# Optimization experiments

Measured on AMD Instinct MI355X. Metric: run time of the kernel, lower is better.

## Reference

```python
import jax, jax.numpy as jnp
import numpy as np

K = 10  # num_objects: top-k humans and top-k objects per image
PERSON_ID = 1
NEG = jnp.float32(-1e30)


def setup_inputs() -> dict:
    key = jax.random.key(0)
    B, N, h, w, D = 8, 100, 96, 96, 768
    kf, ks, k1, k2, k3 = jax.random.split(key, 5)
    features = jax.random.normal(kf, (B, h, w, D), dtype=jnp.float32)
    # valid integer boxes (x1,y1,x2,y2) with x2>x1, y2>y1, inside the feature grid
    rng = np.random.default_rng(0)
    x1 = rng.integers(0, w - 1, (B, N)); x2 = rng.integers(x1 + 1, w + 1)
    y1 = rng.integers(0, h - 1, (B, N)); y2 = rng.integers(y1 + 1, h + 1)
    boxes = jnp.asarray(np.stack([x1, y1, x2, y2], axis=-1).astype(np.int32))
    lab = rng.integers(2, 82, (B, N))
    lab = np.where(rng.random((B, N)) < 0.3, PERSON_ID, lab)
    labels = jnp.asarray(lab.astype(np.int32))
    scores = jax.random.uniform(ks, (B, N), dtype=jnp.float32)
    s = 0.02
    W1 = jax.random.normal(k1, (2 * D, 512), jnp.float32) * s
    b1 = jnp.zeros((512,), jnp.float32)
    W2 = jax.random.normal(k2, (512, 256), jnp.float32) * s
    b2 = jnp.zeros((256,), jnp.float32)
    W3 = jax.random.normal(k3, (256, 117), jnp.float32) * s
    b3 = jnp.zeros((117,), jnp.float32)
    return dict(features=features, boxes=boxes, labels=labels, scores=scores,
                W1=W1, b1=b1, W2=W2, b2=b2, W3=W3, b3=b3)


def _box_mean_pool(features, boxes):
    # Integral image (summed-area table) so all variable-size box means are one gather.
    B, h, w, D = features.shape
    sat = jnp.cumsum(jnp.cumsum(features, axis=1), axis=2)
    sat = jnp.pad(sat, ((0, 0), (1, 0), (1, 0), (0, 0)))  # [B,h+1,w+1,D]
    x1, y1, x2, y2 = boxes[..., 0], boxes[..., 1], boxes[..., 2], boxes[..., 3]
    bi = jnp.arange(B)[:, None]
    box_sum = (sat[bi, y2, x2] - sat[bi, y1, x2]
               - sat[bi, y2, x1] + sat[bi, y1, x1])          # [B,N,D]
    area = ((y2 - y1) * (x2 - x1)).astype(features.dtype)
    return box_sum / area[..., None]


def reference(features, boxes, labels, scores, W1, b1, W2, b2, W3, b3):
    B = features.shape[0]
    D = features.shape[-1]
    pooled = _box_mean_pool(features, boxes)                 # [B,N,D]
    # split by category and take top-K by score (== sort desc + truncate)
    h_sc = jnp.where(labels == PERSON_ID, scores, NEG)
    o_sc = jnp.where(labels != PERSON_ID, scores, NEG)
    hval, hidx = jax.lax.top_k(h_sc, K)                      # [B,K]
    oval, oidx = jax.lax.top_k(o_sc, K)
    h_ok = hval > NEG / 2
    o_ok = oval > NEG / 2
    hfeat = jnp.take_along_axis(pooled, hidx[..., None], axis=1)  # [B,K,D]
    ofeat = jnp.take_along_axis(pooled, oidx[..., None], axis=1)  # [B,K,D]
    # pairwise human-object concat -> [B,K,K,2D]
    pair = jnp.concatenate([
        jnp.broadcast_to(hfeat[:, :, None, :], (B, K, K, D)),
        jnp.broadcast_to(ofeat[:, None, :, :], (B, K, K, D)),
    ], axis=-1)
    x = jax.nn.relu(pair @ W1 + b1)
    x = jax.nn.relu(x @ W2 + b2)
    rel = x @ W3 + b3                                        # [B,K,K,117]
    valid = h_ok[:, :, None] & o_ok[:, None, :]              # [B,K,K] ragged mask
    rel = rel * valid[..., None].astype(rel.dtype)
    return rel, valid
```

## Files before the change

### kernel.cpp

```cpp
#include <hip/hip_runtime.h>
#include <math.h>

#define Bsz 8
#define NBOX 100
#define Hh 96
#define Ww 96
#define Dd 768
#define KK 10
#define C1 512
#define C2 256
#define C3 117

#define OFF_SELIDX 0
#define OFF_OK     160
#define OFF_INV    320
#define OFF_POOLED 512
#define OFF_PART   (512 + 160*Dd)

__global__ void topk_kernel(const int* __restrict__ labels,
                            const float* __restrict__ scores,
                            const int* __restrict__ boxes,
                            int* __restrict__ sel_idx,
                            float* __restrict__ sel_ok,
                            float* __restrict__ inv_area) {
    __shared__ float arr[16][NBOX];
    int tid = threadIdx.x;
    for (int idx = tid; idx < 16 * NBOX; idx += 64) {
        int t = idx / NBOX, n = idx % NBOX;
        int b = t >> 1, c = t & 1;
        int lab = labels[b * NBOX + n];
        bool is_h = (lab == 1);
        bool keep = (c == 0) ? is_h : !is_h;
        arr[t][n] = keep ? scores[b * NBOX + n] : -1e30f;
    }
    __syncthreads();
    if (tid >= 16) return;
    int t = tid, b = t >> 1, c = t & 1;
    for (int k = 0; k < KK; ++k) {
        float bv = -INFINITY; int bi = 0;
        for (int n = 0; n < NBOX; ++n) {
            float v = arr[t][n];
            if (v > bv) { bv = v; bi = n; }
        }
        arr[t][bi] = -INFINITY;
        int s = (b * 2 + c) * KK + k;
        sel_idx[s] = bi;
        sel_ok[s] = (bv > -5e29f) ? 1.0f : 0.0f;
        const int* bx = boxes + (b * NBOX + bi) * 4;
        float area = (float)((bx[3] - bx[1]) * (bx[2] - bx[0]));
        inv_area[s] = 1.0f / area;
    }
}

__global__ void pool_kernel(const float* __restrict__ feat,
                            const int* __restrict__ boxes,
                            const int* __restrict__ sel_idx,
                            float* __restrict__ pooled) {
    int s = blockIdx.x;
    int y = blockIdx.y;
    int b = s / (2 * KK);
    int n = sel_idx[s];
    const int* bx = boxes + (b * NBOX + n) * 4;
    int x1 = bx[0], y1 = bx[1], x2 = bx[2], y2 = bx[3];
    if (y < y1 || y >= y2) return;
    int d4 = threadIdx.x;
    const float4* rowp = (const float4*)feat
        + ((size_t)(b * Hh + y) * Ww) * (Dd / 4) + d4;
    float4 a0 = make_float4(0.f, 0.f, 0.f, 0.f);
    float4 a1 = a0, a2 = a0, a3 = a0;
    int x = x1;
    for (; x + 4 <= x2; x += 4) {
        float4 v0 = rowp[(size_t)(x + 0) * (Dd / 4)];
        float4 v1 = rowp[(size_t)(x + 1) * (Dd / 4)];
        float4 v2 = rowp[(size_t)(x + 2) * (Dd / 4)];
        float4 v3 = rowp[(size_t)(x + 3) * (Dd / 4)];
        a0.x += v0.x; a0.y += v0.y; a0.z += v0.z; a0.w += v0.w;
        a1.x += v1.x; a1.y += v1.y; a1.z += v1.z; a1.w += v1.w;
        a2.x += v2.x; a2.y += v2.y; a2.z += v2.z; a2.w += v2.w;
        a3.x += v3.x; a3.y += v3.y; a3.z += v3.z; a3.w += v3.w;
    }
    for (; x < x2; ++x) {
        float4 v0 = rowp[(size_t)x * (Dd / 4)];
        a0.x += v0.x; a0.y += v0.y; a0.z += v0.z; a0.w += v0.w;
    }
    a0.x += a1.x + a2.x + a3.x;
    a0.y += a1.y + a2.y + a3.y;
    a0.z += a1.z + a2.z + a3.z;
    a0.w += a1.w + a2.w + a3.w;
    float* dst = &pooled[(size_t)s * Dd + d4 * 4];
    atomicAdd(dst + 0, a0.x);
    atomicAdd(dst + 1, a0.y);
    atomicAdd(dst + 2, a0.z);
    atomicAdd(dst + 3, a0.w);
}

__global__ void part_kernel(const float* __restrict__ pooled,
                            const float* __restrict__ inv_area,
                            const float* __restrict__ W1,
                            float* __restrict__ part) {
    __shared__ float pv[KK * Dd];
    int sg = blockIdx.x;
    int o = blockIdx.y * 256 + threadIdx.x;
    for (int idx = threadIdx.x; idx < KK * Dd; idx += 256)
        pv[idx] = pooled[(size_t)sg * KK * Dd + idx];
    __syncthreads();
    int c = sg & 1;
    const float* Wp = W1 + (size_t)(c * Dd) * C1 + o;
    float acc[KK];
#pragma unroll
    for (int j = 0; j < KK; ++j) acc[j] = 0.f;
    for (int d = 0; d < Dd; ++d) {
        float w = Wp[(size_t)d * C1];
#pragma unroll
        for (int j = 0; j < KK; ++j) acc[j] += pv[j * Dd + d] * w;
    }
    for (int j = 0; j < KK; ++j)
        part[(size_t)(sg * KK + j) * C1 + o] = acc[j] * inv_area[sg * KK + j];
}

__global__ void mlp_kernel(const float* __restrict__ part,
                           const float* __restrict__ sel_ok,
                           const float* __restrict__ b1,
                           const float* __restrict__ W2,
                           const float* __restrict__ b2,
                           const float* __restrict__ W3,
                           const float* __restrict__ b3,
                           float* __restrict__ out) {
    __shared__ float x1s[KK][C1];
    __shared__ float x2s[KK][C2];
    int blk = blockIdx.x;
    int b = blk / KK, i = blk % KK;
    const float* hp = part + (size_t)(b * 2 * KK + i) * C1;
    const float* op = part + (size_t)(b * 2 * KK + KK) * C1;
    int tid = threadIdx.x;

    for (int o = tid; o < C1; o += 256) {
        float h = hp[o] + b1[o];
#pragma unroll
        for (int j = 0; j < KK; ++j) {
            float v = h + op[(size_t)j * C1 + o];
            x1s[j][o] = v > 0.f ? v : 0.f;
        }
    }
    __syncthreads();

    {
        int o2 = tid;
        float acc[KK];
        float bb = b2[o2];
#pragma unroll
        for (int j = 0; j < KK; ++j) acc[j] = bb;
        for (int k = 0; k < C1; ++k) {
            float w = W2[(size_t)k * C2 + o2];
#pragma unroll
            for (int j = 0; j < KK; ++j) acc[j] += x1s[j][k] * w;
        }
#pragma unroll
        for (int j = 0; j < KK; ++j) x2s[j][o2] = acc[j] > 0.f ? acc[j] : 0.f;
    }
    __syncthreads();

    float* rel = out;
    float* valid = out + (size_t)Bsz * KK * KK * C3;
    float hok = sel_ok[b * 2 * KK + i];
    if (tid < C3) {
        float acc[KK];
        float bb = b3[tid];
#pragma unroll
        for (int j = 0; j < KK; ++j) acc[j] = bb;
        for (int k = 0; k < C2; ++k) {
            float w = W3[(size_t)k * C3 + tid];
#pragma unroll
            for (int j = 0; j < KK; ++j) acc[j] += x2s[j][k] * w;
        }
        for (int j = 0; j < KK; ++j) {
            float v = hok * sel_ok[b * 2 * KK + KK + j];
            rel[((size_t)(b * KK + i) * KK + j) * C3 + tid] = acc[j] * v;
        }
    }
    if (tid < KK) {
        valid[(size_t)(b * KK + i) * KK + tid] = hok * sel_ok[b * 2 * KK + KK + tid];
    }
}

extern "C" void kernel_launch(void* const* d_in, const int* in_sizes, int n_in,
                              void* d_out, int out_size, void* d_ws, size_t ws_size,
                              hipStream_t stream) {
    const float* feat   = (const float*)d_in[0];
    const int*   boxes  = (const int*)d_in[1];
    const int*   labels = (const int*)d_in[2];
    const float* scores = (const float*)d_in[3];
    const float* W1     = (const float*)d_in[4];
    const float* b1     = (const float*)d_in[5];
    const float* W2     = (const float*)d_in[6];
    const float* b2     = (const float*)d_in[7];
    const float* W3     = (const float*)d_in[8];
    const float* b3     = (const float*)d_in[9];

    float* ws       = (float*)d_ws;
    int*   sel_idx  = (int*)(ws + OFF_SELIDX);
    float* sel_ok   = ws + OFF_OK;
    float* inv_area = ws + OFF_INV;
    float* pooled   = ws + OFF_POOLED;
    float* part     = ws + OFF_PART;

    hipMemsetAsync(pooled, 0, sizeof(float) * 160 * Dd, stream);
    topk_kernel<<<1, 64, 0, stream>>>(labels, scores, boxes, sel_idx, sel_ok, inv_area);
    pool_kernel<<<dim3(160, 96), 192, 0, stream>>>(feat, boxes, sel_idx, pooled);
    part_kernel<<<dim3(16, 2), 256, 0, stream>>>(pooled, inv_area, W1, part);
    mlp_kernel<<<Bsz * KK, 256, 0, stream>>>(part, sel_ok, b1, W2, b2, W3, b3, (float*)d_out);
}
```

Baseline: 584.2 us.

## Replace atomic pooling with per-chunk partial sums and wave-parallel top-k

Pool blocks now each cover two rows and write a float4 partial sum to a dedicated slot instead of doing atomicAdds into a zeroed buffer. The memset goes away, and part_kernel reduces the 48 partials per box while loading. Top-k moves from 16 serial threads to 16 wavefronts that use shuffle-based argmax reductions. The cost is extra partial-buffer traffic (160×48×768 floats), a serial 48-step reduction in part_kernel, and a __syncthreads on every top-k iteration.

Measured after the change: 535.1 us. -8.4%, faster.

```diff
diff --git a/kernel.cpp b/kernel.cpp
--- a/kernel.cpp
+++ b/kernel.cpp
@@ -10,12 +10,13 @@
 #define C1 512
 #define C2 256
 #define C3 117
+#define NCHUNK 48
 
 #define OFF_SELIDX 0
 #define OFF_OK     160
 #define OFF_INV    320
-#define OFF_POOLED 512
-#define OFF_PART   (512 + 160*Dd)
+#define OFF_PART   512
+#define OFF_PARTIAL (512 + 160*C1)
 
 __global__ void topk_kernel(const int* __restrict__ labels,
                             const float* __restrict__ scores,
@@ -25,84 +26,101 @@
                             float* __restrict__ inv_area) {
     __shared__ float arr[16][NBOX];
     int tid = threadIdx.x;
-    for (int idx = tid; idx < 16 * NBOX; idx += 64) {
-        int t = idx / NBOX, n = idx % NBOX;
+    for (int idx = tid; idx < 16 * NBOX; idx += 1024) {
+        int t = idx / NBOX, n = idx - t * NBOX;
         int b = t >> 1, c = t & 1;
         int lab = labels[b * NBOX + n];
-        bool is_h = (lab == 1);
-        bool keep = (c == 0) ? is_h : !is_h;
+        bool keep = (c == 0) ? (lab == 1) : (lab != 1);
         arr[t][n] = keep ? scores[b * NBOX + n] : -1e30f;
     }
     __syncthreads();
-    if (tid >= 16) return;
-    int t = tid, b = t >> 1, c = t & 1;
+    int w = tid >> 6, lane = tid & 63;
+    int b = w >> 1;
     for (int k = 0; k < KK; ++k) {
-        float bv = -INFINITY; int bi = 0;
-        for (int n = 0; n < NBOX; ++n) {
-            float v = arr[t][n];
-            if (v > bv) { bv = v; bi = n; }
-        }
-        arr[t][bi] = -INFINITY;
-        int s = (b * 2 + c) * KK + k;
-        sel_idx[s] = bi;
-        sel_ok[s] = (bv > -5e29f) ? 1.0f : 0.0f;
-        const int* bx = boxes + (b * NBOX + bi) * 4;
-        float area = (float)((bx[3] - bx[1]) * (bx[2] - bx[0]));
-        inv_area[s] = 1.0f / area;
+        float bv = arr[w][lane]; int bi = lane;
+        if (lane + 64 < NBOX) {
+            float v = arr[w][lane + 64];
+            if (v > bv) { bv = v; bi = lane + 64; }
+        }
+#pragma unroll
+        for (int off = 32; off >= 1; off >>= 1) {
+            float ov = __shfl_xor(bv, off);
+            int   oi = __shfl_xor(bi, off);
+            if (ov > bv || (ov == bv && oi < bi)) { bv = ov; bi = oi; }
+        }
+        if (lane == 0) {
+            arr[w][bi] = -INFINITY;
+            int s = w * KK + k;
+            sel_idx[s] = bi;
+            sel_ok[s] = (bv > -5e29f) ? 1.0f : 0.0f;
+            const int* bx = boxes + (b * NBOX + bi) * 4;
+            inv_area[s] = 1.0f / (float)((bx[3] - bx[1]) * (bx[2] - bx[0]));
+        }
+        __syncthreads();
     }
 }
 
 __global__ void pool_kernel(const float* __restrict__ feat,
                             const int* __restrict__ boxes,
                             const int* __restrict__ sel_idx,
-                            float* __restrict__ pooled) {
-    int s = blockIdx.x;
-    int y = blockIdx.y;
+                            float* __restrict__ partial) {
+    int s = blockIdx.x, yc = blockIdx.y;
     int b = s / (2 * KK);
     int n = sel_idx[s];
     const int* bx = boxes + (b * NBOX + n) * 4;
     int x1 = bx[0], y1 = bx[1], x2 = bx[2], y2 = bx[3];
-    if (y < y1 || y >= y2) return;
     int d4 = threadIdx.x;
-    const float4* rowp = (const float4*)feat
-        + ((size_t)(b * Hh + y) * Ww) * (Dd / 4) + d4;
     float4 a0 = make_float4(0.f, 0.f, 0.f, 0.f);
     float4 a1 = a0, a2 = a0, a3 = a0;
-    int x = x1;
-    for (; x + 4 <= x2; x += 4) {
-        float4 v0 = rowp[(size_t)(x + 0) * (Dd / 4)];
-        float4 v1 = rowp[(size_t)(x + 1) * (Dd / 4)];
-        float4 v2 = rowp[(size_t)(x + 2) * (Dd / 4)];
-        float4 v3 = rowp[(size_t)(x + 3) * (Dd / 4)];
-        a0.x += v0.x; a0.y += v0.y; a0.z += v0.z; a0.w += v0.w;
-        a1.x += v1.x; a1.y += v1.y; a1.z += v1.z; a1.w += v1.w;
-        a2.x += v2.x; a2.y += v2.y; a2.z += v2.z; a2.w += v2.w;
-        a3.x += v3.x; a3.y += v3.y; a3.z += v3.z; a3.w += v3.w;
-    }
-    for (; x < x2; ++x) {
-        float4 v0 = rowp[(size_t)x * (Dd / 4)];
-        a0.x += v0.x; a0.y += v0.y; a0.z += v0.z; a0.w += v0.w;
-    }
-    a0.x += a1.x + a2.x + a3.x;
-    a0.y += a1.y + a2.y + a3.y;
-    a0.z += a1.z + a2.z + a3.z;
-    a0.w += a1.w + a2.w + a3.w;
-    float* dst = &pooled[(size_t)s * Dd + d4 * 4];
-    atomicAdd(dst + 0, a0.x);
-    atomicAdd(dst + 1, a0.y);
-    atomicAdd(dst + 2, a0.z);
-    atomicAdd(dst + 3, a0.w);
-}
-
-__global__ void part_kernel(const float* __restrict__ pooled,
+    int y0 = y1 + 2 * yc;
+    if (y0 < y2) {
+        int ye = min(y0 + 2, y2);
+        const float4* feat4 = (const float4*)feat;
+        for (int y = y0; y < ye; ++y) {
+            const float4* rowp = feat4 + ((size_t)(b * Hh + y) * Ww) * (Dd / 4) + d4;
+            int x = x1;
+            for (; x + 4 <= x2; x += 4) {
+                float4 v0 = rowp[(size_t)(x + 0) * (Dd / 4)];
+                float4 v1 = rowp[(size_t)(x + 1) * (Dd / 4)];
+                float4 v2 = rowp[(size_t)(x + 2) * (Dd / 4)];
+                float4 v3 = rowp[(size_t)(x + 3) * (Dd / 4)];
+                a0.x += v0.x; a0.y += v0.y; a0.z += v0.z; a0.w += v0.w;
+                a1.x += v1.x; a1.y += v1.y; a1.z += v1.z; a1.w += v1.w;
+                a2.x += v2.x; a2.y += v2.y; a2.z += v2.z; a2.w += v2.w;
+                a3.x += v3.x; a3.y += v3.y; a3.z += v3.z; a3.w += v3.w;
+            }
+            for (; x < x2; ++x) {
+                float4 v0 = rowp[(size_t)x * (Dd / 4)];
+                a0.x += v0.x; a0.y += v0.y; a0.z += v0.z; a0.w += v0.w;
+            }
+        }
+        a0.x += a1.x + a2.x + a3.x;
+        a0.y += a1.y + a2.y + a3.y;
+        a0.z += a1.z + a2.z + a3.z;
+        a0.w += a1.w + a2.w + a3.w;
+    }
+    ((float4*)partial)[((size_t)s * NCHUNK + yc) * (Dd / 4) + d4] = a0;
+}
+
+__global__ void part_kernel(const float* __restrict__ partial,
                             const float* __restrict__ inv_area,
                             const float* __restrict__ W1,
                             float* __restrict__ part) {
     __shared__ float pv[KK * Dd];
     int sg = blockIdx.x;
     int o = blockIdx.y * 256 + threadIdx.x;
-    for (int idx = threadIdx.x; idx < KK * Dd; idx += 256)
-        pv[idx] = pooled[(size_t)sg * KK * Dd + idx];
+    const float4* p4 = (const float4*)partial;
+    float4* pv4 = (float4*)pv;
+    for (int idx = threadIdx.x; idx < KK * (Dd / 4); idx += 256) {
+        int j = idx / (Dd / 4), d4 = idx - j * (Dd / 4);
+        const float4* src = p4 + ((size_t)(sg * KK + j) * NCHUNK) * (Dd / 4) + d4;
+        float4 acc = make_float4(0.f, 0.f, 0.f, 0.f);
+        for (int yc = 0; yc < NCHUNK; ++yc) {
+            float4 v = src[(size_t)yc * (Dd / 4)];
+            acc.x += v.x; acc.y += v.y; acc.z += v.z; acc.w += v.w;
+        }
+        pv4[idx] = acc;
+    }
     __syncthreads();
     int c = sg & 1;
     const float* Wp = W1 + (size_t)(c * Dd) * C1 + o;
@@ -201,12 +219,11 @@
     int*   sel_idx  = (int*)(ws + OFF_SELIDX);
     float* sel_ok   = ws + OFF_OK;
     float* inv_area = ws + OFF_INV;
-    float* pooled   = ws + OFF_POOLED;
     float* part     = ws + OFF_PART;
-
-    hipMemsetAsync(pooled, 0, sizeof(float) * 160 * Dd, stream);
-    topk_kernel<<<1, 64, 0, stream>>>(labels, scores, boxes, sel_idx, sel_ok, inv_area);
-    pool_kernel<<<dim3(160, 96), 192, 0, stream>>>(feat, boxes, sel_idx, pooled);
-    part_kernel<<<dim3(16, 2), 256, 0, stream>>>(pooled, inv_area, W1, part);
+    float* partial  = ws + OFF_PARTIAL;
+
+    topk_kernel<<<1, 1024, 0, stream>>>(labels, scores, boxes, sel_idx, sel_ok, inv_area);
+    pool_kernel<<<dim3(160, NCHUNK), 192, 0, stream>>>(feat, boxes, sel_idx, partial);
+    part_kernel<<<dim3(16, 2), 256, 0, stream>>>(partial, inv_area, W1, part);
     mlp_kernel<<<Bsz * KK, 256, 0, stream>>>(part, sel_ok, b1, W2, b2, W3, b3, (float*)d_out);
 }
```
